# Performance work log

Hardware: AMD Instinct MI355X
Metric: run time of the kernel (lower is better)

The kernel has to match this reference:

```python
import jax, jax.numpy as jnp
import numpy as np

N = 50000      # num_nodes
R = 8          # num_relations
FIN = 128      # in_channels
H = 128        # hidden_channels
E = 800000     # num_edges (avg degree 16)


def _xavier(key, shape):
    fan_in, fan_out = shape[-2], shape[-1]
    lim = np.sqrt(6.0 / (fan_in + fan_out)).astype(np.float32)
    return jax.random.uniform(key, shape, jnp.float32, -lim, lim)


def setup_inputs() -> dict:
    key = jax.random.key(0)
    ks = jax.random.split(key, 10)
    return {
        "x": jax.random.normal(ks[0], (N, FIN), jnp.float32),
        "edge_index": jax.random.randint(ks[1], (2, E), 0, N, jnp.int32),
        "edge_type": jax.random.randint(ks[2], (E,), 0, R, jnp.int32),
        "rel_w0": _xavier(ks[3], (R, FIN, H)),
        "root_w0": _xavier(ks[4], (FIN, H)),
        "bias0": jnp.zeros((H,), jnp.float32),
        "rel_w1": _xavier(ks[5], (R, H, H)),
        "root_w1": _xavier(ks[6], (H, H)),
        "bias1": jnp.zeros((H,), jnp.float32),
        "rel_emb": _xavier(ks[7], (R, H)),
    }


def _rgcn_conv(x, src, dst, etype, rel_w, root_w, bias):
    # RGCNConv (PyG, aggr='mean'): out_i = root(x_i) + sum_r W_r * mean_{j in N_r(i)} x_j
    n = x.shape[0]
    seg = dst * R + etype                                   # fused (node, relation) segment id
    msgs = x[src]                                           # [E, F] gather
    sums = jax.ops.segment_sum(msgs, seg, num_segments=n * R)
    cnt = jax.ops.segment_sum(jnp.ones((src.shape[0], 1), x.dtype), seg, num_segments=n * R)
    mean = (sums / jnp.maximum(cnt, 1.0)).reshape(n, R, -1)  # [N, R, F]
    return jnp.einsum('nrf,rfh->nh', mean, rel_w) + x @ root_w + bias


def reference(x, edge_index, edge_type, rel_w0, root_w0, bias0,
              rel_w1, root_w1, bias1, rel_emb):
    src, dst = edge_index[0], edge_index[1]
    h = _rgcn_conv(x, src, dst, edge_type, rel_w0, root_w0, bias0)
    h = jax.nn.relu(h)  # dropout in eval mode (identity)
    h = _rgcn_conv(h, src, dst, edge_type, rel_w1, root_w1, bias1)
    return (h, rel_emb)
```

## Files before the change

### kernel.cpp

```cpp
#include <hip/hip_runtime.h>

typedef unsigned short ushort_t;
typedef __attribute__((ext_vector_type(8))) short short8;
typedef __attribute__((ext_vector_type(4))) float f32x4;
typedef __attribute__((ext_vector_type(4))) int int4v;

#define RNUM 8
#define FDIM 128
#define KDIM 1152

__device__ __forceinline__ float bf2f(ushort_t u) {
    union { unsigned int i; float f; } x;
    x.i = ((unsigned int)u) << 16;
    return x.f;
}
__device__ __forceinline__ ushort_t f2bf(float f) {
    union { float f; unsigned int i; } x;
    x.f = f;
    unsigned int u = x.i;
    u += 0x7fffu + ((u >> 16) & 1u);
    return (ushort_t)(u >> 16);
}

__device__ __forceinline__ void gl_lds16(const void* g, void* s) {
    __builtin_amdgcn_global_load_lds(
        (const __attribute__((address_space(1))) unsigned int*)g,
        (__attribute__((address_space(3))) unsigned int*)s, 16, 0, 0);
}


__global__ void zero_kernel(int* p, int n) {
    int i = blockIdx.x * 256 + threadIdx.x;
    if (i < n) p[i] = 0;
}

__global__ void hist_kernel(const int* __restrict__ dst, const int* __restrict__ et,
                            int* cnt, int E) {
    int i = blockIdx.x * 256 + threadIdx.x;
    if (i < E) atomicAdd(&cnt[dst[i] * RNUM + et[i]], 1);
}

__global__ __launch_bounds__(256) void scan_a(const int* __restrict__ cnt,
                                              int* __restrict__ part,
                                              int* __restrict__ bsum, int n) {
    __shared__ int sd[256];
    int tid = threadIdx.x;
    int base = blockIdx.x * 1024 + tid * 4;
    int v0 = (base + 0 < n) ? cnt[base + 0] : 0;
    int v1 = (base + 1 < n) ? cnt[base + 1] : 0;
    int v2 = (base + 2 < n) ? cnt[base + 2] : 0;
    int v3 = (base + 3 < n) ? cnt[base + 3] : 0;
    int tot = v0 + v1 + v2 + v3;
    sd[tid] = tot;
    __syncthreads();
    for (int off = 1; off < 256; off <<= 1) {
        int t = (tid >= off) ? sd[tid - off] : 0;
        __syncthreads();
        sd[tid] += t;
        __syncthreads();
    }
    int run = sd[tid] - tot;
    if (base + 0 < n) part[base + 0] = run; run += v0;
    if (base + 1 < n) part[base + 1] = run; run += v1;
    if (base + 2 < n) part[base + 2] = run; run += v2;
    if (base + 3 < n) part[base + 3] = run;
    if (tid == 255) bsum[blockIdx.x] = sd[255];
}

__global__ __launch_bounds__(512) void scan_b(int* bsum, int nb) {
    __shared__ int sd[512];
    int tid = threadIdx.x;
    int v = (tid < nb) ? bsum[tid] : 0;
    sd[tid] = v;
    __syncthreads();
    for (int off = 1; off < 512; off <<= 1) {
        int t = (tid >= off) ? sd[tid - off] : 0;
        __syncthreads();
        sd[tid] += t;
        __syncthreads();
    }
    if (tid < nb) bsum[tid] = sd[tid] - v;
}

__global__ void scan_c(int* row_ptr, int* cursor, const int* __restrict__ bsum,
                       int n, int total) {
    int i = blockIdx.x * 256 + threadIdx.x;
    if (i < n) {
        int v = row_ptr[i] + bsum[i >> 10];
        row_ptr[i] = v;
        cursor[i] = v;
    }
    if (i == 0) row_ptr[n] = total;
}

__global__ void scatter_kernel(const int* __restrict__ src, const int* __restrict__ dst,
                               const int* __restrict__ et, int* cursor,
                               int* __restrict__ ssrc, int E) {
    int i = blockIdx.x * 256 + threadIdx.x;
    if (i < E) {
        int seg = dst[i] * RNUM + et[i];
        int pos = atomicAdd(&cursor[seg], 1);
        ssrc[pos] = src[i];
    }
}


__global__ __launch_bounds__(256) void transpose_w(const float* __restrict__ rel_w,
                                                   const float* __restrict__ root_w,
                                                   ushort_t* __restrict__ Wt) {
    int r = blockIdx.x;
    const float* src = (r < 8) ? (rel_w + r * 16384) : root_w;
    __shared__ ushort_t t[128 * 130];
    for (int idx = threadIdx.x; idx < 16384; idx += 256)
        t[(idx >> 7) * 130 + (idx & 127)] = f2bf(src[idx]);
    __syncthreads();
    ushort_t* d = Wt + r * 16384;
    for (int idx = threadIdx.x; idx < 16384; idx += 256)
        d[idx] = t[(idx & 127) * 130 + (idx >> 7)];
}


__global__ void cast_x(const float* __restrict__ x, ushort_t* __restrict__ Mx, int total) {
    int i = (blockIdx.x * 256 + threadIdx.x) * 8;
    if (i >= total) return;
    float4 v0 = *(const float4*)(x + i);
    float4 v1 = *(const float4*)(x + i + 4);
    ushort_t o[8] = {f2bf(v0.x), f2bf(v0.y), f2bf(v0.z), f2bf(v0.w),
                     f2bf(v1.x), f2bf(v1.y), f2bf(v1.z), f2bf(v1.w)};
    int row = i >> 7, col = i & 127;
    *(int4v*)(Mx + (size_t)row * KDIM + 1024 + col) = *(int4v*)o;
}


__global__ __launch_bounds__(256) void seg_mean(const int* __restrict__ row_ptr,
                                                const int* __restrict__ ssrc,
                                                ushort_t* Mx, int NSEG) {
    int t = blockIdx.x * 256 + threadIdx.x;
    int seg = t >> 4;
    int l16 = t & 15;
    if (seg >= NSEG) return;
    int s0 = row_ptr[seg], s1 = row_ptr[seg + 1];
    float acc0[8], acc1[8];
#pragma unroll
    for (int k = 0; k < 8; ++k) { acc0[k] = 0.f; acc1[k] = 0.f; }
    const ushort_t* gbase = Mx + 1024 + (size_t)l16 * 8;
    int e = s0;
    for (; e + 1 < s1; e += 2) {
        int j0 = ssrc[e], j1 = ssrc[e + 1];
        int4v v0 = *(const int4v*)(gbase + (size_t)j0 * KDIM);
        int4v v1 = *(const int4v*)(gbase + (size_t)j1 * KDIM);
        ushort_t* p0 = (ushort_t*)&v0;
        ushort_t* p1 = (ushort_t*)&v1;
#pragma unroll
        for (int k = 0; k < 8; ++k) { acc0[k] += bf2f(p0[k]); acc1[k] += bf2f(p1[k]); }
    }
    if (e < s1) {
        int j0 = ssrc[e];
        int4v v0 = *(const int4v*)(gbase + (size_t)j0 * KDIM);
        ushort_t* p0 = (ushort_t*)&v0;
#pragma unroll
        for (int k = 0; k < 8; ++k) acc0[k] += bf2f(p0[k]);
    }
    float sc = (s1 > s0) ? 1.0f / (float)(s1 - s0) : 0.f;
    ushort_t ov[8];
#pragma unroll
    for (int k = 0; k < 8; ++k) ov[k] = f2bf((acc0[k] + acc1[k]) * sc);
    *(int4v*)(Mx + (size_t)(seg >> 3) * KDIM + (seg & 7) * 128 + l16 * 8) = *(int4v*)ov;
}


template <bool FINAL>
__global__ __launch_bounds__(256) void rgcn_gemm(
    const ushort_t* Mx, const ushort_t* __restrict__ Wt,
    const float* __restrict__ bias, float* __restrict__ outF,
    ushort_t* MxOut, int N) {
    __shared__ ushort_t As[128 * 128];
    __shared__ ushort_t Bs[128 * 128];
    int tid = threadIdx.x;
    int wid = tid >> 6, lane = tid & 63;
    int l16 = lane & 15, q = lane >> 4;
    int nodeBase = blockIdx.x * 128;

    f32x4 acc[2][8];
#pragma unroll
    for (int rt = 0; rt < 2; ++rt)
#pragma unroll
        for (int ct = 0; ct < 8; ++ct) acc[rt][ct] = (f32x4){0.f, 0.f, 0.f, 0.f};

    for (int r = 0; r < 9; ++r) {
        __syncthreads();
#pragma unroll
        for (int i = 0; i < 8; ++i) {
            int L = i * 256 + tid;
            int row = L >> 4;
            int c = (L & 15) ^ (row & 15);
            gl_lds16(Mx + (size_t)(nodeBase + row) * KDIM + r * 128 + c * 8,
                     (char*)As + (size_t)L * 16);
            gl_lds16(Wt + r * 16384 + row * 128 + c * 8,
                     (char*)Bs + (size_t)L * 16);
        }
        __syncthreads();
#pragma unroll
        for (int s = 0; s < 4; ++s) {
            int pos = ((s * 4 + q) ^ l16) * 16;
            short8 a0 = *(const short8*)((const char*)As + ((2 * wid + 0) * 16 + l16) * 256 + pos);
            short8 a1 = *(const short8*)((const char*)As + ((2 * wid + 1) * 16 + l16) * 256 + pos);
#pragma unroll
            for (int ct = 0; ct < 8; ++ct) {
                short8 b = *(const short8*)((const char*)Bs + (ct * 16 + l16) * 256 + pos);
                acc[0][ct] = __builtin_amdgcn_mfma_f32_16x16x32_bf16(a0, b, acc[0][ct], 0, 0, 0);
                acc[1][ct] = __builtin_amdgcn_mfma_f32_16x16x32_bf16(a1, b, acc[1][ct], 0, 0, 0);
            }
        }
    }
#pragma unroll
    for (int rt = 0; rt < 2; ++rt) {
#pragma unroll
        for (int ct = 0; ct < 8; ++ct) {
            int h = ct * 16 + l16;
            float bv = bias[h];
#pragma unroll
            for (int reg = 0; reg < 4; ++reg) {
                int node = nodeBase + (2 * wid + rt) * 16 + q * 4 + reg;
                if (node < N) {
                    float v = acc[rt][ct][reg] + bv;
                    if (FINAL) {
                        outF[(size_t)node * FDIM + h] = v;
                    } else {
                        v = fmaxf(v, 0.f);
                        MxOut[(size_t)node * KDIM + 1024 + h] = f2bf(v);
                    }
                }
            }
        }
    }
}

__global__ void copy_emb(const float* __restrict__ e, float* __restrict__ out, int n) {
    int i = blockIdx.x * 256 + threadIdx.x;
    if (i < n) out[i] = e[i];
}


extern "C" void kernel_launch(void* const* d_in, const int* in_sizes, int n_in,
                              void* d_out, int out_size, void* d_ws, size_t ws_size,
                              hipStream_t stream) {
    const float* x        = (const float*)d_in[0];
    const int* edge_index = (const int*)d_in[1];
    const int* edge_type  = (const int*)d_in[2];
    const float* rel_w0   = (const float*)d_in[3];
    const float* root_w0  = (const float*)d_in[4];
    const float* bias0    = (const float*)d_in[5];
    const float* rel_w1   = (const float*)d_in[6];
    const float* root_w1  = (const float*)d_in[7];
    const float* bias1    = (const float*)d_in[8];
    const float* rel_emb  = (const float*)d_in[9];

    int N = in_sizes[0] / FDIM;
    int E = in_sizes[1] / 2;
    int NSEG = N * RNUM;
    const int* src = edge_index;
    const int* dst = edge_index + E;

    int nb_gemm = (N + 127) / 128;
    int NPAD = nb_gemm * 128;

    char* w = (char*)d_ws;
    auto alloc = [&](size_t bytes) -> char* {
        char* p = w;
        w += (bytes + 255) & ~(size_t)255;
        return p;
    };
    int* cnt     = (int*)alloc((size_t)NSEG * 4);
    int* row_ptr = (int*)alloc((size_t)(NSEG + 1) * 4);
    int* bsum    = (int*)alloc(1024 * 4);
    int* ssrc    = (int*)alloc((size_t)E * 4);
    ushort_t* Wt = (ushort_t*)alloc((size_t)2 * 9 * 16384 * 2);
    ushort_t* Mx = (ushort_t*)alloc((size_t)NPAD * KDIM * 2);
    int* cursor = cnt;
    (void)ws_size; (void)n_in; (void)out_size;

    int nb_seg  = (NSEG + 255) / 256;
    int nb_E    = (E + 255) / 256;
    int nb_scan = (NSEG + 1023) / 1024;
    int nb_mean = (NSEG * 16) / 256;
    int nb_cast = (N * FDIM) / (256 * 8);

    zero_kernel<<<nb_seg, 256, 0, stream>>>(cnt, NSEG);
    hist_kernel<<<nb_E, 256, 0, stream>>>(dst, edge_type, cnt, E);
    scan_a<<<nb_scan, 256, 0, stream>>>(cnt, row_ptr, bsum, NSEG);
    scan_b<<<1, 512, 0, stream>>>(bsum, nb_scan);
    scan_c<<<nb_seg, 256, 0, stream>>>(row_ptr, cursor, bsum, NSEG, E);
    scatter_kernel<<<nb_E, 256, 0, stream>>>(src, dst, edge_type, cursor, ssrc, E);
    transpose_w<<<9, 256, 0, stream>>>(rel_w0, root_w0, Wt);
    transpose_w<<<9, 256, 0, stream>>>(rel_w1, root_w1, Wt + 9 * 16384);
    cast_x<<<nb_cast, 256, 0, stream>>>(x, Mx, N * FDIM);

    seg_mean<<<nb_mean, 256, 0, stream>>>(row_ptr, ssrc, Mx, NSEG);
    rgcn_gemm<false><<<nb_gemm, 256, 0, stream>>>(Mx, Wt, bias0, nullptr, Mx, N);
    seg_mean<<<nb_mean, 256, 0, stream>>>(row_ptr, ssrc, Mx, NSEG);
    rgcn_gemm<true><<<nb_gemm, 256, 0, stream>>>(Mx, Wt + 9 * 16384, bias1,
                                                 (float*)d_out, nullptr, N);
    copy_emb<<<4, 256, 0, stream>>>(rel_emb, (float*)d_out + (size_t)N * FDIM,
                                    in_sizes[9]);
}
```

Measured before the change: 349.7 us.

## Replace CSR build with atomic-exchange linked lists per segment

```diff
diff --git a/kernel.cpp b/kernel.cpp
--- a/kernel.cpp
+++ b/kernel.cpp
@@ -29,78 +29,17 @@
 }
 
 
-__global__ void zero_kernel(int* p, int n) {
+__global__ void init_head(int* __restrict__ head, int n) {
     int i = blockIdx.x * 256 + threadIdx.x;
-    if (i < n) p[i] = 0;
-}
-
-__global__ void hist_kernel(const int* __restrict__ dst, const int* __restrict__ et,
-                            int* cnt, int E) {
-    int i = blockIdx.x * 256 + threadIdx.x;
-    if (i < E) atomicAdd(&cnt[dst[i] * RNUM + et[i]], 1);
-}
-
-__global__ __launch_bounds__(256) void scan_a(const int* __restrict__ cnt,
-                                              int* __restrict__ part,
-                                              int* __restrict__ bsum, int n) {
-    __shared__ int sd[256];
-    int tid = threadIdx.x;
-    int base = blockIdx.x * 1024 + tid * 4;
-    int v0 = (base + 0 < n) ? cnt[base + 0] : 0;
-    int v1 = (base + 1 < n) ? cnt[base + 1] : 0;
-    int v2 = (base + 2 < n) ? cnt[base + 2] : 0;
-    int v3 = (base + 3 < n) ? cnt[base + 3] : 0;
-    int tot = v0 + v1 + v2 + v3;
-    sd[tid] = tot;
-    __syncthreads();
-    for (int off = 1; off < 256; off <<= 1) {
-        int t = (tid >= off) ? sd[tid - off] : 0;
-        __syncthreads();
-        sd[tid] += t;
-        __syncthreads();
-    }
-    int run = sd[tid] - tot;
-    if (base + 0 < n) part[base + 0] = run; run += v0;
-    if (base + 1 < n) part[base + 1] = run; run += v1;
-    if (base + 2 < n) part[base + 2] = run; run += v2;
-    if (base + 3 < n) part[base + 3] = run;
-    if (tid == 255) bsum[blockIdx.x] = sd[255];
-}
-
-__global__ __launch_bounds__(512) void scan_b(int* bsum, int nb) {
-    __shared__ int sd[512];
-    int tid = threadIdx.x;
-    int v = (tid < nb) ? bsum[tid] : 0;
-    sd[tid] = v;
-    __syncthreads();
-    for (int off = 1; off < 512; off <<= 1) {
-        int t = (tid >= off) ? sd[tid - off] : 0;
-        __syncthreads();
-        sd[tid] += t;
-        __syncthreads();
-    }
-    if (tid < nb) bsum[tid] = sd[tid] - v;
-}
-
-__global__ void scan_c(int* row_ptr, int* cursor, const int* __restrict__ bsum,
-                       int n, int total) {
-    int i = blockIdx.x * 256 + threadIdx.x;
-    if (i < n) {
-        int v = row_ptr[i] + bsum[i >> 10];
-        row_ptr[i] = v;
-        cursor[i] = v;
-    }
-    if (i == 0) row_ptr[n] = total;
-}
-
-__global__ void scatter_kernel(const int* __restrict__ src, const int* __restrict__ dst,
-                               const int* __restrict__ et, int* cursor,
-                               int* __restrict__ ssrc, int E) {
+    if (i < n) head[i] = -1;
+}
+
+__global__ void link_kernel(const int* __restrict__ dst, const int* __restrict__ et,
+                            int* head, int* __restrict__ nxt, int E) {
     int i = blockIdx.x * 256 + threadIdx.x;
     if (i < E) {
         int seg = dst[i] * RNUM + et[i];
-        int pos = atomicAdd(&cursor[seg], 1);
-        ssrc[pos] = src[i];
+        nxt[i] = atomicExch(&head[seg], i);
     }
 }
 
@@ -132,39 +71,34 @@
 }
 
 
-__global__ __launch_bounds__(256) void seg_mean(const int* __restrict__ row_ptr,
-                                                const int* __restrict__ ssrc,
+__global__ __launch_bounds__(256) void seg_mean(const int* __restrict__ head,
+                                                const int* __restrict__ nxt,
+                                                const int* __restrict__ esrc,
                                                 ushort_t* Mx, int NSEG) {
     int t = blockIdx.x * 256 + threadIdx.x;
     int seg = t >> 4;
     int l16 = t & 15;
     if (seg >= NSEG) return;
-    int s0 = row_ptr[seg], s1 = row_ptr[seg + 1];
-    float acc0[8], acc1[8];
-#pragma unroll
-    for (int k = 0; k < 8; ++k) { acc0[k] = 0.f; acc1[k] = 0.f; }
+    float acc[8];
+#pragma unroll
+    for (int k = 0; k < 8; ++k) acc[k] = 0.f;
     const ushort_t* gbase = Mx + 1024 + (size_t)l16 * 8;
-    int e = s0;
-    for (; e + 1 < s1; e += 2) {
-        int j0 = ssrc[e], j1 = ssrc[e + 1];
-        int4v v0 = *(const int4v*)(gbase + (size_t)j0 * KDIM);
-        int4v v1 = *(const int4v*)(gbase + (size_t)j1 * KDIM);
-        ushort_t* p0 = (ushort_t*)&v0;
-        ushort_t* p1 = (ushort_t*)&v1;
-#pragma unroll
-        for (int k = 0; k < 8; ++k) { acc0[k] += bf2f(p0[k]); acc1[k] += bf2f(p1[k]); }
-    }
-    if (e < s1) {
-        int j0 = ssrc[e];
-        int4v v0 = *(const int4v*)(gbase + (size_t)j0 * KDIM);
-        ushort_t* p0 = (ushort_t*)&v0;
-#pragma unroll
-        for (int k = 0; k < 8; ++k) acc0[k] += bf2f(p0[k]);
-    }
-    float sc = (s1 > s0) ? 1.0f / (float)(s1 - s0) : 0.f;
+    int cnt = 0;
+    int j = head[seg];
+    while (j >= 0) {
+        int s = esrc[j];
+        int jn = nxt[j];
+        int4v v = *(const int4v*)(gbase + (size_t)s * KDIM);
+        ushort_t* p = (ushort_t*)&v;
+#pragma unroll
+        for (int k = 0; k < 8; ++k) acc[k] += bf2f(p[k]);
+        ++cnt;
+        j = jn;
+    }
+    float sc = (cnt > 0) ? 1.0f / (float)cnt : 0.f;
     ushort_t ov[8];
 #pragma unroll
-    for (int k = 0; k < 8; ++k) ov[k] = f2bf((acc0[k] + acc1[k]) * sc);
+    for (int k = 0; k < 8; ++k) ov[k] = f2bf(acc[k] * sc);
     *(int4v*)(Mx + (size_t)(seg >> 3) * KDIM + (seg & 7) * 128 + l16 * 8) = *(int4v*)ov;
 }
 
@@ -271,34 +205,26 @@
         w += (bytes + 255) & ~(size_t)255;
         return p;
     };
-    int* cnt     = (int*)alloc((size_t)NSEG * 4);
-    int* row_ptr = (int*)alloc((size_t)(NSEG + 1) * 4);
-    int* bsum    = (int*)alloc(1024 * 4);
-    int* ssrc    = (int*)alloc((size_t)E * 4);
+    int* head    = (int*)alloc((size_t)NSEG * 4);
+    int* nxt     = (int*)alloc((size_t)E * 4);
     ushort_t* Wt = (ushort_t*)alloc((size_t)2 * 9 * 16384 * 2);
     ushort_t* Mx = (ushort_t*)alloc((size_t)NPAD * KDIM * 2);
-    int* cursor = cnt;
     (void)ws_size; (void)n_in; (void)out_size;
 
     int nb_seg  = (NSEG + 255) / 256;
     int nb_E    = (E + 255) / 256;
-    int nb_scan = (NSEG + 1023) / 1024;
     int nb_mean = (NSEG * 16) / 256;
     int nb_cast = (N * FDIM) / (256 * 8);
 
-    zero_kernel<<<nb_seg, 256, 0, stream>>>(cnt, NSEG);
-    hist_kernel<<<nb_E, 256, 0, stream>>>(dst, edge_type, cnt, E);
-    scan_a<<<nb_scan, 256, 0, stream>>>(cnt, row_ptr, bsum, NSEG);
-    scan_b<<<1, 512, 0, stream>>>(bsum, nb_scan);
-    scan_c<<<nb_seg, 256, 0, stream>>>(row_ptr, cursor, bsum, NSEG, E);
-    scatter_kernel<<<nb_E, 256, 0, stream>>>(src, dst, edge_type, cursor, ssrc, E);
+    init_head<<<nb_seg, 256, 0, stream>>>(head, NSEG);
+    link_kernel<<<nb_E, 256, 0, stream>>>(dst, edge_type, head, nxt, E);
     transpose_w<<<9, 256, 0, stream>>>(rel_w0, root_w0, Wt);
     transpose_w<<<9, 256, 0, stream>>>(rel_w1, root_w1, Wt + 9 * 16384);
     cast_x<<<nb_cast, 256, 0, stream>>>(x, Mx, N * FDIM);
 
-    seg_mean<<<nb_mean, 256, 0, stream>>>(row_ptr, ssrc, Mx, NSEG);
+    seg_mean<<<nb_mean, 256, 0, stream>>>(head, nxt, src, Mx, NSEG);
     rgcn_gemm<false><<<nb_gemm, 256, 0, stream>>>(Mx, Wt, bias0, nullptr, Mx, N);
-    seg_mean<<<nb_mean, 256, 0, stream>>>(row_ptr, ssrc, Mx, NSEG);
+    seg_mean<<<nb_mean, 256, 0, stream>>>(head, nxt, src, Mx, NSEG);
     rgcn_gemm<true><<<nb_gemm, 256, 0, stream>>>(Mx, Wt + 9 * 16384, bias1,
                                                  (float*)d_out, nullptr, N);
     copy_emb<<<4, 256, 0, stream>>>(rel_emb, (float*)d_out + (size_t)N * FDIM,
```

Measured after the change: 333.3 us. 4.7% less time.
